# Performance work log

Measured on AMD Instinct MI355X. Metric: run time of the kernel, lower is better.

The kernel has to match this reference:

```python
import jax, jax.numpy as jnp
import numpy as np
from jax.scipy.special import logsumexp

EPS_OT = 0.05      # self.eps in AttentionOT
MAX_ITER = 100     # Sinkhorn max_iter (torch early-stops; at convergence results match)


def _l2norm(x):
    # F.normalize(x, dim=-1, p=2) with eps=1e-12
    return x / jnp.maximum(jnp.linalg.norm(x, axis=-1, keepdims=True), 1e-12)


def _sinkhorn(Cmat, mu, nu, eps):
    # Cmat: (BK, M, N), mu: (BK, M), nu: (BK, N)
    log_mu = jnp.log(mu + 1e-8)
    log_nu = jnp.log(nu + 1e-8)

    def kern(u, v):
        # log Boltzmann kernel: (-C + u_i + v_j) / eps, shape (BK, M, N)
        return (-Cmat + u[..., :, None] + v[..., None, :]) / eps

    def step(carry, _):
        u, v = carry
        u = eps * (log_mu - logsumexp(kern(u, v), axis=2)) + u
        v = eps * (log_nu - logsumexp(kern(u, v), axis=1)) + v
        return (u, v), None

    u0 = jnp.zeros_like(mu)
    v0 = jnp.zeros_like(nu)
    (u, v), _ = jax.lax.scan(jax.checkpoint(step), (u0, v0), None, length=MAX_ITER)
    return jnp.exp(kern(u, v))  # transport plan T, (BK, M, N)


def setup_inputs() -> dict:
    key = jax.random.key(0)
    Nq, M, B, K, C = 64, 16, 8, 256, 512
    ks = jax.random.split(key, 8)
    s = 1.0 / np.sqrt(C)  # torch nn.Linear default init bound
    return {
        "xq": jax.random.normal(ks[0], (Nq, M, B, C), jnp.float32),
        "xk": jax.random.normal(ks[1], (B, K, C), jnp.float32),
        "xv": jax.random.normal(ks[2], (B, K, C), jnp.float32),
        "Wq": jax.random.uniform(ks[3], (C, C), jnp.float32, -s, s),
        "Wk": jax.random.uniform(ks[4], (C, C), jnp.float32, -s, s),
        "Wv": jax.random.uniform(ks[5], (C, C), jnp.float32, -s, s),
        "Wp": jax.random.uniform(ks[6], (C, C), jnp.float32, -s, s),
        "bp": jax.random.uniform(ks[7], (C,), jnp.float32, -s, s),
    }


def reference(xq, xk, xv, Wq, Wk, Wv, Wp, bp):
    Nq, M, B, C = xq.shape
    K = xk.shape[1]
    # projections (qkv_bias=False; proj has bias). dropout probs are 0 -> identity.
    q = _l2norm(xq @ Wq.T)          # (Nq, M, B, C)
    kk = _l2norm(xk @ Wk.T)         # (B, K, C)
    v = xv @ Wv.T                   # (B, K, C)
    # torch: einsum('bkc,nmbc->bnkm') then permute(0,2,3,1) -> (B,K,M,Nq)
    sim = jnp.einsum('bkc,nmbc->bkmn', kk, q).reshape(B * K, M, Nq)
    wdist = 1.0 - sim
    mu = jnp.full((B * K, M), 1.0 / M, dtype=sim.dtype)
    nu = jnp.full((B * K, Nq), 1.0 / Nq, dtype=sim.dtype)
    T = _sinkhorn(wdist, mu, nu, EPS_OT)            # (B*K, M, Nq)
    score_map = (M * Nq * sim * T).reshape(B, K, M, Nq)
    attn = T.reshape(B, K, M, Nq).transpose(3, 0, 1, 2)  # (Nq, B, K, M)
    x = jnp.einsum('nbkm,bkc->nmbc', attn, v)            # (Nq, M, B, C)
    x = x @ Wp.T + bp
    return x, score_map
```

## Files before the change

kernel.cpp:

```cpp
#include <hip/hip_runtime.h>


typedef short   short8  __attribute__((ext_vector_type(8)));
typedef float   floatx4 __attribute__((ext_vector_type(4)));
typedef unsigned int uint2e __attribute__((ext_vector_type(2)));

static __device__ __forceinline__ float fastrcp(float x) {
    return __builtin_amdgcn_rcpf(x);
}
static __device__ __forceinline__ unsigned short f2bf(float f) {
    union { float f; unsigned u; } c; c.f = f;
    unsigned r = c.u + 0x7FFF + ((c.u >> 16) & 1);
    return (unsigned short)(r >> 16);
}
static __device__ __forceinline__ float bf2f(unsigned short h) {
    union { unsigned u; float f; } c; c.u = (unsigned)h << 16;
    return c.f;
}

static __device__ __forceinline__ void gll16(const unsigned short* g, short* l) {
    __builtin_amdgcn_global_load_lds(
        (const __attribute__((address_space(1))) void*)g,
        (__attribute__((address_space(3))) void*)l, 16, 0, 0);
}

#if __has_builtin(__builtin_amdgcn_permlane16_swap)
static __device__ __forceinline__ float xadd16(float s) {
    uint2e r = __builtin_amdgcn_permlane16_swap(
        __float_as_uint(s), __float_as_uint(s), false, false);
    return __uint_as_float(r.x) + __uint_as_float(r.y);
}
#else
static __device__ __forceinline__ float xadd16(float s) {
    return s + __shfl_xor(s, 16, 64);
}
#endif
#if __has_builtin(__builtin_amdgcn_permlane32_swap)
static __device__ __forceinline__ float xadd32(float s) {
    uint2e r = __builtin_amdgcn_permlane32_swap(
        __float_as_uint(s), __float_as_uint(s), false, false);
    return __uint_as_float(r.x) + __uint_as_float(r.y);
}
#else
static __device__ __forceinline__ float xadd32(float s) {
    return s + __shfl_xor(s, 32, 64);
}
#endif

#define RRI(x, C) __builtin_amdgcn_update_dpp(0, (x), (C), 0xf, 0xf, true)
#define RRF(x, C) __int_as_float(RRI(__float_as_int(x), (C)))
#define GATH16(d, s) do { d[0] = (s);                                        \
    d[1]  = RRF((s), 0x121); d[2]  = RRF((s), 0x122);                        \
    d[3]  = RRF((s), 0x123); d[4]  = RRF((s), 0x124);                        \
    d[5]  = RRF((s), 0x125); d[6]  = RRF((s), 0x126);                        \
    d[7]  = RRF((s), 0x127); d[8]  = RRF((s), 0x128);                        \
    d[9]  = RRF((s), 0x129); d[10] = RRF((s), 0x12a);                        \
    d[11] = RRF((s), 0x12b); d[12] = RRF((s), 0x12c);                        \
    d[13] = RRF((s), 0x12d); d[14] = RRF((s), 0x12e);                        \
    d[15] = RRF((s), 0x12f); } while (0)

__global__ __launch_bounds__(256) void prep(
    const float* __restrict__ xq, const float* __restrict__ xk,
    const float* __restrict__ xv, const float* __restrict__ Wq,
    const float* __restrict__ Wk, const float* __restrict__ Wv,
    const float* __restrict__ Wp,
    unsigned short* __restrict__ xqh, unsigned short* __restrict__ xql,
    unsigned short* __restrict__ xkh, unsigned short* __restrict__ xkl,
    unsigned short* __restrict__ xvb,
    unsigned short* __restrict__ wqh, unsigned short* __restrict__ wql,
    unsigned short* __restrict__ wkh, unsigned short* __restrict__ wkl,
    unsigned short* __restrict__ wvb, unsigned short* __restrict__ wpb)
{
    const int b = blockIdx.x;
    const float* src; unsigned short *dh, *dl; long base;
    if (b < 4096)      { src = xq; dh = xqh; dl = xql;     base = (long)b * 256; }
    else if (b < 5120) { src = xk; dh = xkh; dl = xkl;     base = (long)(b - 4096) * 256; }
    else if (b < 6144) { src = xv; dh = xvb; dl = nullptr; base = (long)(b - 5120) * 256; }
    else if (b < 6400) { src = Wq; dh = wqh; dl = wql;     base = (long)(b - 6144) * 256; }
    else if (b < 6656) { src = Wk; dh = wkh; dl = wkl;     base = (long)(b - 6400) * 256; }
    else if (b < 6912) { src = Wv; dh = wvb; dl = nullptr; base = (long)(b - 6656) * 256; }
    else               { src = Wp; dh = wpb; dl = nullptr; base = (long)(b - 6912) * 256; }
    const long i = base + threadIdx.x;
    float4 v = ((const float4*)src)[i];
    ushort4 h;
    h.x = f2bf(v.x); h.y = f2bf(v.y); h.z = f2bf(v.z); h.w = f2bf(v.w);
    ((ushort4*)dh)[i] = h;
    if (dl) {
        ushort4 l;
        l.x = f2bf(v.x - bf2f(h.x)); l.y = f2bf(v.y - bf2f(h.y));
        l.z = f2bf(v.z - bf2f(h.z)); l.w = f2bf(v.w - bf2f(h.w));
        ((ushort4*)dl)[i] = l;
    }
}

__global__ __launch_bounds__(256, 3) void gemm_qkv2(
    const unsigned short* __restrict__ xqh, const unsigned short* __restrict__ xql,
    const unsigned short* __restrict__ xkh, const unsigned short* __restrict__ xkl,
    const unsigned short* __restrict__ xvb,
    const unsigned short* __restrict__ wqh, const unsigned short* __restrict__ wql,
    const unsigned short* __restrict__ wkh, const unsigned short* __restrict__ wkl,
    const unsigned short* __restrict__ wvb,
    unsigned short* __restrict__ qh, unsigned short* __restrict__ ql,
    unsigned short* __restrict__ kh, unsigned short* __restrict__ kl,
    unsigned short* __restrict__ vt)
{
    __shared__ __align__(16) short LB[24576];

    const int bt = blockIdx.x;
    const unsigned short *Ah, *Al, *Bh, *Bl;
    int seg, arow0;
    if (bt < 128)      { Ah = xqh; Al = xql; Bh = wqh; Bl = wql; arow0 = bt * 64;         seg = 0; }
    else if (bt < 160) { Ah = xkh; Al = xkl; Bh = wkh; Bl = wkl; arow0 = (bt - 128) * 64; seg = 1; }
    else               { Ah = xvb; Al = xvb; Bh = wvb; Bl = wvb; arow0 = (bt - 160) * 64; seg = 2; }
    const bool split = (seg != 2);

    const int tid  = threadIdx.x;
    const int lane = tid & 63, wv = tid >> 6;
    const int wc = wv * 32;
    const int j0 = blockIdx.y * 128;

    floatx4 acc[4][2];
#pragma unroll
    for (int i = 0; i < 4; i++)
#pragma unroll
        for (int j = 0; j < 2; j++) acc[i][j] = {0.f, 0.f, 0.f, 0.f};

    const int lrow = lane >> 2;
    const int lch  = (lane & 3) * 8;
    const int gra  = 16 * wv;
    const int grb  = 32 * wv;
    const long gA0 = (long)(arow0 + gra + lrow) * 512 + lch;
    const long gB0 = (long)(j0    + grb + lrow) * 512 + lch;

    const int fr = lane & 15, fq = (lane >> 4) * 8;

#define QKV_STAGE(d, k0) do {                                                 \
        short* bb = LB + (d) * 12288;                                         \
        gll16(Ah + gA0 + (k0),            bb + gra * 32);                     \
        gll16(Bh + gB0 + (k0),            bb + 4096 + grb * 32);              \
        gll16(Bh + gB0 + (k0) + 16 * 512, bb + 4096 + (grb + 16) * 32);       \
        if (split) {                                                          \
            gll16(Al + gA0 + (k0),            bb + 2048 + gra * 32);          \
            gll16(Bl + gB0 + (k0),            bb + 8192 + grb * 32);          \
            gll16(Bl + gB0 + (k0) + 16 * 512, bb + 8192 + (grb + 16) * 32);   \
        }                                                                     \
    } while (0)

    QKV_STAGE(0, 0);
    __syncthreads();

#pragma unroll 2
    for (int t = 0; t < 16; t++) {
        const int cur = t & 1;
        if (t < 15) QKV_STAGE(cur ^ 1, (t + 1) * 32);
        const short* base = LB + cur * 12288;
        short8 ah[4], bh[2];
#pragma unroll
        for (int i = 0; i < 4; i++)
            ah[i] = *(const short8*)&base[(i * 16 + fr) * 32 + fq];
#pragma unroll
        for (int j = 0; j < 2; j++)
            bh[j] = *(const short8*)&base[4096 + (wc + j * 16 + fr) * 32 + fq];
        if (split) {
            short8 al[4], bl[2];
#pragma unroll
            for (int i = 0; i < 4; i++)
                al[i] = *(const short8*)&base[2048 + (i * 16 + fr) * 32 + fq];
#pragma unroll
            for (int j = 0; j < 2; j++)
                bl[j] = *(const short8*)&base[8192 + (wc + j * 16 + fr) * 32 + fq];
#pragma unroll
            for (int i = 0; i < 4; i++)
#pragma unroll
                for (int j = 0; j < 2; j++) {
                    acc[i][j] = __builtin_amdgcn_mfma_f32_16x16x32_bf16(ah[i], bh[j], acc[i][j], 0, 0, 0);
                    acc[i][j] = __builtin_amdgcn_mfma_f32_16x16x32_bf16(ah[i], bl[j], acc[i][j], 0, 0, 0);
                    acc[i][j] = __builtin_amdgcn_mfma_f32_16x16x32_bf16(al[i], bh[j], acc[i][j], 0, 0, 0);
                }
        } else {
#pragma unroll
            for (int i = 0; i < 4; i++)
#pragma unroll
                for (int j = 0; j < 2; j++)
                    acc[i][j] = __builtin_amdgcn_mfma_f32_16x16x32_bf16(ah[i], bh[j], acc[i][j], 0, 0, 0);
        }
        __syncthreads();
    }
#undef QKV_STAGE

    const int cr = (lane >> 4) * 4, cc = lane & 15;
    if (seg == 2) {
        short (*S2)[72] = (short(*)[72])LB;
#pragma unroll
        for (int i = 0; i < 4; i++)
#pragma unroll
            for (int j = 0; j < 2; j++)
#pragma unroll
                for (int r = 0; r < 4; r++)
                    S2[wc + j * 16 + cc][i * 16 + cr + r] =
                        (short)f2bf(acc[i][j][r]);
        __syncthreads();
        const int orow = tid >> 1;
        const int os   = (tid & 1) * 32;
        unsigned short* dst = vt + (long)(arow0 >> 8) * 131072
                            + (long)(j0 + orow) * 256 + (arow0 & 255) + os;
#pragma unroll
        for (int c8 = 0; c8 < 4; c8++)
            *(short8*)(dst + c8 * 8) = *(const short8*)&S2[orow][os + c8 * 8];
    } else {
#pragma unroll
        for (int i = 0; i < 4; i++)
#pragma unroll
            for (int j = 0; j < 2; j++) {
                const int gj = j0 + wc + j * 16 + cc;
#pragma unroll
                for (int r = 0; r < 4; r++) {
                    const int gi = arow0 + i * 16 + cr + r;
                    const float v = acc[i][j][r];
                    const unsigned short h = f2bf(v);
                    const unsigned short lo = f2bf(v - bf2f(h));
                    if (seg == 0) {
                        const long orow = (long)((gi & 7) * 1024 + ((gi >> 3) & 15) * 64 + (gi >> 7));
                        qh[orow * 512 + gj] = h;
                        ql[orow * 512 + gj] = lo;
                    } else {
                        kh[(long)gi * 512 + gj] = h;
                        kl[(long)gi * 512 + gj] = lo;
                    }
                }
            }
    }
}

__global__ __launch_bounds__(256) void gemm_sim64(
    const short* __restrict__ Ah, const short* __restrict__ Al,
    const short* __restrict__ Bh, const short* __restrict__ Bl,
    float* __restrict__ Out)
{
    const int z = blockIdx.z;
    Ah += (long)z * 131072;  Al += (long)z * 131072;
    Bh += (long)z * 524288;  Bl += (long)z * 524288;
    Out += (long)z * 262144;

    __shared__ __align__(16) short Ash[64][40];
    __shared__ __align__(16) short Asl[64][40];
    __shared__ __align__(16) short Bsh[64][40];
    __shared__ __align__(16) short Bsl[64][40];
    __shared__ float sRA[64];
    __shared__ float sRB[64];

    const int tid  = threadIdx.x;
    const int lane = tid & 63, wv = tid >> 6;
    const int wr = (wv >> 1) * 32, wc = (wv & 1) * 32;
    const int i0 = blockIdx.x * 64, j0 = blockIdx.y * 64;

    floatx4 acc[2][2];
#pragma unroll
    for (int i = 0; i < 2; i++)
#pragma unroll
        for (int j = 0; j < 2; j++) acc[i][j] = {0.f, 0.f, 0.f, 0.f};

    const int sr = tid >> 2, sch = (tid & 3) * 8;
    const int fr = lane & 15, fq = (lane >> 4) * 8;

    float ssqA = 0.0f, ssqB = 0.0f;

    for (int k0 = 0; k0 < 512; k0 += 32) {
        const long ao = (long)(i0 + sr) * 512 + k0 + sch;
        const long bo = (long)(j0 + sr) * 512 + k0 + sch;
        const short8 vah = *(const short8*)(Ah + ao);
        const short8 val_ = *(const short8*)(Al + ao);
        const short8 vbh = *(const short8*)(Bh + bo);
        const short8 vbl = *(const short8*)(Bl + bo);
        *(short8*)&Ash[sr][sch] = vah;
        *(short8*)&Asl[sr][sch] = val_;
        *(short8*)&Bsh[sr][sch] = vbh;
        *(short8*)&Bsl[sr][sch] = vbl;
#pragma unroll
        for (int e = 0; e < 8; e++) {
            const float va = bf2f((unsigned short)vah[e]) + bf2f((unsigned short)val_[e]);
            const float vb = bf2f((unsigned short)vbh[e]) + bf2f((unsigned short)vbl[e]);
            ssqA = fmaf(va, va, ssqA);
            ssqB = fmaf(vb, vb, ssqB);
        }
        __syncthreads();
        short8 ah[2], al[2], bh[2], bl[2];
#pragma unroll
        for (int i = 0; i < 2; i++) {
            ah[i] = *(const short8*)&Ash[wr + i * 16 + fr][fq];
            al[i] = *(const short8*)&Asl[wr + i * 16 + fr][fq];
        }
#pragma unroll
        for (int j = 0; j < 2; j++) {
            bh[j] = *(const short8*)&Bsh[wc + j * 16 + fr][fq];
            bl[j] = *(const short8*)&Bsl[wc + j * 16 + fr][fq];
        }
#pragma unroll
        for (int i = 0; i < 2; i++)
#pragma unroll
            for (int j = 0; j < 2; j++) {
                acc[i][j] = __builtin_amdgcn_mfma_f32_16x16x32_bf16(ah[i], bh[j], acc[i][j], 0, 0, 0);
                acc[i][j] = __builtin_amdgcn_mfma_f32_16x16x32_bf16(ah[i], bl[j], acc[i][j], 0, 0, 0);
                acc[i][j] = __builtin_amdgcn_mfma_f32_16x16x32_bf16(al[i], bh[j], acc[i][j], 0, 0, 0);
            }
        __syncthreads();
    }

    ssqA += __shfl_xor(ssqA, 1, 64);  ssqA += __shfl_xor(ssqA, 2, 64);
    ssqB += __shfl_xor(ssqB, 1, 64);  ssqB += __shfl_xor(ssqB, 2, 64);
    if ((tid & 3) == 0) {
        sRA[sr] = 1.0f / fmaxf(sqrtf(ssqA), 1e-12f);
        sRB[sr] = 1.0f / fmaxf(sqrtf(ssqB), 1e-12f);
    }
    __syncthreads();

    const int cr = (lane >> 4) * 4, cc = lane & 15;
#pragma unroll
    for (int i = 0; i < 2; i++)
#pragma unroll
        for (int j = 0; j < 2; j++) {
            const int lc = wc + j * 16 + cc;
            const float sq = sRB[lc];
            const int gj = j0 + lc;
#pragma unroll
            for (int r = 0; r < 4; r++) {
                const int lr = wr + i * 16 + cr + r;
                Out[(long)(i0 + lr) * 1024 + gj] = acc[i][j][r] * sRA[lr] * sq;
            }
        }
}

template <bool BIAS, bool OPERM, bool OUT_BF16>
__global__ __launch_bounds__(256, 2) void gemm_bf16_v2(
    const unsigned short* __restrict__ A, const unsigned short* __restrict__ B,
    const float* __restrict__ bias, void* __restrict__ OutV,
    int Kdim, int lda, int ldb, int ldo, long sA, long sB, long sO)
{
    __shared__ __align__(16) short LB[12288];

    const int tid  = threadIdx.x;
    const int lane = tid & 63, wv = tid >> 6;
    const int wc = wv * 32;
    const int i0 = blockIdx.x * 64, j0 = blockIdx.y * 128;

    floatx4 acc[4][2];
#pragma unroll
    for (int i = 0; i < 4; i++)
#pragma unroll
        for (int j = 0; j < 2; j++) acc[i][j] = {0.f, 0.f, 0.f, 0.f};

    const unsigned short* pa = A + (long)blockIdx.z * sA;
    const unsigned short* pb = B + (long)blockIdx.z * sB;

    const int lrow = lane >> 2;
    const int lch  = (lane & 3) * 8;
    const int gra  = 16 * wv;
    const int grb  = 32 * wv;
    const long gA0 = (long)(i0 + gra + lrow) * lda + lch;
    const long gB0 = (long)(j0 + grb + lrow) * ldb + lch;

    const int fr = lane & 15, fq = (lane >> 4) * 8;

#define BF2_STAGE(d, k0) do {                                                 \
        short* bb = LB + (d) * 6144;                                          \
        gll16(pa + gA0 + (k0),             bb + gra * 32);                    \
        gll16(pb + gB0 + (k0),             bb + 2048 + grb * 32);             \
        gll16(pb + gB0 + (k0) + 16 * ldb,  bb + 2048 + (grb + 16) * 32);      \
    } while (0)

    const int nt = Kdim >> 5;
    BF2_STAGE(0, 0);
    __syncthreads();

#pragma unroll 2
    for (int t = 0; t < nt; t++) {
        const int cur = t & 1;
        if (t < nt - 1) BF2_STAGE(cur ^ 1, (t + 1) * 32);
        const short* base = LB + cur * 6144;
        short8 af[4], bf[2];
#pragma unroll
        for (int i = 0; i < 4; i++)
            af[i] = *(const short8*)&base[(i * 16 + fr) * 32 + fq];
#pragma unroll
        for (int j = 0; j < 2; j++)
            bf[j] = *(const short8*)&base[2048 + (wc + j * 16 + fr) * 32 + fq];
#pragma unroll
        for (int i = 0; i < 4; i++)
#pragma unroll
            for (int j = 0; j < 2; j++)
                acc[i][j] = __builtin_amdgcn_mfma_f32_16x16x32_bf16(af[i], bf[j], acc[i][j], 0, 0, 0);
        __syncthreads();
    }
#undef BF2_STAGE

    float* Of = nullptr; unsigned short* Ob = nullptr;
    if constexpr (OUT_BF16) Ob = (unsigned short*)OutV + (long)blockIdx.z * sO;
    else                    Of = (float*)OutV + (long)blockIdx.z * sO;
    const int cr = (lane >> 4) * 4, cc = lane & 15;
#pragma unroll
    for (int i = 0; i < 4; i++) {
#pragma unroll
        for (int j = 0; j < 2; j++) {
            const int gj = j0 + wc + j * 16 + cc;
            float bb = 0.0f;
            if constexpr (BIAS) bb = bias[gj];
#pragma unroll
            for (int r = 0; r < 4; r++) {
                const int gi = i0 + i * 16 + cr + r;
                float v = acc[i][j][r] + bb;
                long idx;
                if constexpr (OPERM)
                    idx = (long)((gi & 63) * 128 + ((gi >> 6) & 15) * 8 + (gi >> 10)) * ldo + gj;
                else
                    idx = (long)gi * ldo + gj;
                if constexpr (OUT_BF16) Ob[idx] = f2bf(v);
                else                    Of[idx] = v;
            }
        }
    }
}

__global__ __launch_bounds__(256, 2) void sinkhorn5(
    const float* __restrict__ sim, float* __restrict__ score,
    unsigned short* __restrict__ Tt)
{
    const int lane = threadIdx.x & 63;
    const int bk   = blockIdx.x * 4 + (threadIdx.x >> 6);
    const float* S = sim + (long)bk * 1024;
    const int m = lane & 15, g = lane >> 4;

    int idx[16];
    idx[0] = m;
    idx[1]  = RRI(m, 0x121); idx[2]  = RRI(m, 0x122); idx[3]  = RRI(m, 0x123);
    idx[4]  = RRI(m, 0x124); idx[5]  = RRI(m, 0x125); idx[6]  = RRI(m, 0x126);
    idx[7]  = RRI(m, 0x127); idx[8]  = RRI(m, 0x128); idx[9]  = RRI(m, 0x129);
    idx[10] = RRI(m, 0x12a); idx[11] = RRI(m, 0x12b); idx[12] = RRI(m, 0x12c);
    idx[13] = RRI(m, 0x12d); idx[14] = RRI(m, 0x12e); idx[15] = RRI(m, 0x12f);

    float K1[16], K2R[16], sv[16];
#pragma unroll
    for (int j = 0; j < 16; j++) {
        K1[j] = __expf((S[m * 64 + g * 16 + idx[j]] - 1.0f) * 20.0f);
        const float s_ = S[idx[j] * 64 + lane];
        sv[j]  = s_;
        K2R[j] = __expf((s_ - 1.0f) * 20.0f);
    }

    const float muP = 0.0625f + 1e-8f;
    const float nuP = 0.015625f + 1e-8f;
    float b = 1.0f;
    float aB[16], bB[16];
#pragma unroll
    for (int j = 0; j < 16; j++) bB[j] = 1.0f;

#pragma unroll 1
    for (int it = 0; it < 100; it++) {
        float s0 = 0, s1 = 0, s2 = 0, s3 = 0;
#pragma unroll
        for (int j = 0; j < 4; j++) {
            s0 = fmaf(K1[j],      bB[j],      s0);
            s1 = fmaf(K1[4 + j],  bB[4 + j],  s1);
            s2 = fmaf(K1[8 + j],  bB[8 + j],  s2);
            s3 = fmaf(K1[12 + j], bB[12 + j], s3);
        }
        float s = (s0 + s1) + (s2 + s3);
        s = xadd16(s);
        s = xadd32(s);
        const float a = muP * fastrcp(s);
        GATH16(aB, a);
        float t0 = 0, t1 = 0, t2 = 0, t3 = 0;
#pragma unroll
        for (int j = 0; j < 4; j++) {
            t0 = fmaf(K2R[j],      aB[j],      t0);
            t1 = fmaf(K2R[4 + j],  aB[4 + j],  t1);
            t2 = fmaf(K2R[8 + j],  aB[8 + j],  t2);
            t3 = fmaf(K2R[12 + j], aB[12 + j], t3);
        }
        const float bp_ = b;
        b = nuP * fastrcp((t0 + t1) + (t2 + t3));
        GATH16(bB, b);
        const int conv = __builtin_fabsf(b - bp_) <= 1e-5f * __builtin_fabsf(b);
        if (__all(conv)) break;
    }

    float* Sc = score + (long)bk * 1024;
    unsigned short* Tp = Tt + (long)(bk >> 8) * 262144 + (bk & 255);
#pragma unroll
    for (int j = 0; j < 16; j++) {
        const int row = idx[j];
        const float Tv = aB[j] * K2R[j] * b;
        Sc[row * 64 + lane] = 1024.0f * sv[j] * Tv;
        Tp[(long)(row * 64 + lane) * 256] = f2bf(Tv);
    }
}

extern "C" void kernel_launch(void* const* d_in, const int* in_sizes, int n_in,
                              void* d_out, int out_size, void* d_ws, size_t ws_size,
                              hipStream_t stream)
{
    (void)in_sizes; (void)n_in; (void)out_size; (void)ws_size;
    const float* xq = (const float*)d_in[0];
    const float* xk = (const float*)d_in[1];
    const float* xv = (const float*)d_in[2];
    const float* Wq = (const float*)d_in[3];
    const float* Wk = (const float*)d_in[4];
    const float* Wv = (const float*)d_in[5];
    const float* Wp = (const float*)d_in[6];
    const float* bp = (const float*)d_in[7];

    float* out_x     = (float*)d_out;
    float* out_score = out_x + 8192L * 512;

    char* W = (char*)d_ws;
    const long MB = 1 << 20;
    unsigned short* qh   = (unsigned short*)(W + 0);
    unsigned short* ql   = (unsigned short*)(W + 8 * MB);
    unsigned short* xq_h = (unsigned short*)(W + 16 * MB);
    float*          simb = (float*)(W + 16 * MB);
    unsigned short* xq_l = (unsigned short*)(W + 24 * MB);
    unsigned short* xpre = (unsigned short*)(W + 24 * MB);
    unsigned short* xk_h = (unsigned short*)(W + 32 * MB);
    unsigned short* xk_l = (unsigned short*)(W + 34 * MB);
    unsigned short* Tt   = (unsigned short*)(W + 32 * MB);
    unsigned short* xv_b = (unsigned short*)(W + 36 * MB);
    unsigned short* kh   = (unsigned short*)(W + 38 * MB);
    unsigned short* kl   = (unsigned short*)(W + 40 * MB);
    unsigned short* vt   = (unsigned short*)(W + 42 * MB);
    unsigned short* wqh  = (unsigned short*)(W + 44 * MB);
    unsigned short* wql  = (unsigned short*)(W + 44 * MB + 1 * 524288);
    unsigned short* wkh  = (unsigned short*)(W + 44 * MB + 2 * 524288);
    unsigned short* wkl  = (unsigned short*)(W + 44 * MB + 3 * 524288);
    unsigned short* wvb  = (unsigned short*)(W + 44 * MB + 4 * 524288);
    unsigned short* wpb  = (unsigned short*)(W + 44 * MB + 5 * 524288);

    const dim3 blk(256);

    prep<<<7168, blk, 0, stream>>>(xq, xk, xv, Wq, Wk, Wv, Wp,
                                   xq_h, xq_l, xk_h, xk_l, xv_b,
                                   wqh, wql, wkh, wkl, wvb, wpb);

    gemm_qkv2<<<dim3(192, 4), blk, 0, stream>>>(
        xq_h, xq_l, xk_h, xk_l, xv_b, wqh, wql, wkh, wkl, wvb,
        qh, ql, kh, kl, vt);

    gemm_sim64<<<dim3(4, 16, 8), blk, 0, stream>>>(
        (const short*)kh, (const short*)kl, (const short*)qh, (const short*)ql,
        simb);

    sinkhorn5<<<512, blk, 0, stream>>>(simb, out_score, Tt);

    gemm_bf16_v2<false, false, true><<<dim3(16, 4, 8), blk, 0, stream>>>(
        Tt, vt, nullptr, xpre,
        256, 256, 256, 512, 262144, 131072, 524288);

    gemm_bf16_v2<true, true, false><<<dim3(128, 4), blk, 0, stream>>>(
        xpre, wpb, bp, out_x,
        512, 512, 512, 512, 0, 0, 0);
}
```

Before: 180.4 us.

## Fuse row norms into QKV epilogue and double-buffer sim GEMM with LDS DMA

The q and k row sums of squares now accumulate in the projection GEMM epilogue through shuffles and atomics into a buffer that prep zeroes. The sim GEMM therefore no longer computes them per tile. The sim GEMM also moves from register-staged LDS loads to global_load_lds direct loads with a double buffer, which lets loads overlap MFMA work. This adds atomic traffic and more LDS per block (launch bounds now allow 2 blocks). Each epilogue thread also recomputes rsqrt from global memory.

```diff
diff --git a/kernel.cpp b/kernel.cpp
--- a/kernel.cpp
+++ b/kernel.cpp
@@ -69,7 +69,8 @@
     unsigned short* __restrict__ xvb,
     unsigned short* __restrict__ wqh, unsigned short* __restrict__ wql,
     unsigned short* __restrict__ wkh, unsigned short* __restrict__ wkl,
-    unsigned short* __restrict__ wvb, unsigned short* __restrict__ wpb)
+    unsigned short* __restrict__ wvb, unsigned short* __restrict__ wpb,
+    float* __restrict__ rs)
 {
     const int b = blockIdx.x;
     const float* src; unsigned short *dh, *dl; long base;
@@ -91,6 +92,10 @@
         l.z = f2bf(v.z - bf2f(h.z)); l.w = f2bf(v.w - bf2f(h.w));
         ((ushort4*)dl)[i] = l;
     }
+    if (b == 7167) {
+#pragma unroll
+        for (int ii = 0; ii < 40; ii++) rs[threadIdx.x + ii * 256] = 0.0f;
+    }
 }
 
 __global__ __launch_bounds__(256, 3) void gemm_qkv2(
@@ -102,7 +107,7 @@
     const unsigned short* __restrict__ wvb,
     unsigned short* __restrict__ qh, unsigned short* __restrict__ ql,
     unsigned short* __restrict__ kh, unsigned short* __restrict__ kl,
-    unsigned short* __restrict__ vt)
+    unsigned short* __restrict__ vt, float* __restrict__ rs)
 {
     __shared__ __align__(16) short LB[24576];
 
@@ -208,6 +213,9 @@
         for (int c8 = 0; c8 < 4; c8++)
             *(short8*)(dst + c8 * 8) = *(const short8*)&S2[orow][os + c8 * 8];
     } else {
+        float prow[16];
+#pragma unroll
+        for (int ii = 0; ii < 16; ii++) prow[ii] = 0.0f;
 #pragma unroll
         for (int i = 0; i < 4; i++)
 #pragma unroll
@@ -219,6 +227,8 @@
                     const float v = acc[i][j][r];
                     const unsigned short h = f2bf(v);
                     const unsigned short lo = f2bf(v - bf2f(h));
+                    const float vv = bf2f(h) + bf2f(lo);
+                    prow[i * 4 + r] = fmaf(vv, vv, prow[i * 4 + r]);
                     if (seg == 0) {
                         const long orow = (long)((gi & 7) * 1024 + ((gi >> 3) & 15) * 64 + (gi >> 7));
                         qh[orow * 512 + gj] = h;
@@ -229,25 +239,41 @@
                     }
                 }
             }
-    }
-}
-
-__global__ __launch_bounds__(256) void gemm_sim64(
-    const short* __restrict__ Ah, const short* __restrict__ Al,
-    const short* __restrict__ Bh, const short* __restrict__ Bl,
-    float* __restrict__ Out)
+#pragma unroll
+        for (int i = 0; i < 4; i++)
+#pragma unroll
+            for (int r = 0; r < 4; r++) {
+                float p = prow[i * 4 + r];
+                p += __shfl_xor(p, 1, 64);
+                p += __shfl_xor(p, 2, 64);
+                p += __shfl_xor(p, 4, 64);
+                p += __shfl_xor(p, 8, 64);
+                if (cc == 0) {
+                    const int gi = arow0 + i * 16 + cr + r;
+                    long ri;
+                    if (seg == 0)
+                        ri = (long)((gi & 7) * 1024 + ((gi >> 3) & 15) * 64 + (gi >> 7));
+                    else
+                        ri = 8192 + (long)gi;
+                    atomicAdd(rs + ri, p);
+                }
+            }
+    }
+}
+
+__global__ __launch_bounds__(256, 2) void gemm_sim64(
+    const unsigned short* __restrict__ Ah, const unsigned short* __restrict__ Al,
+    const unsigned short* __restrict__ Bh, const unsigned short* __restrict__ Bl,
+    float* __restrict__ Out, const float* __restrict__ rs)
 {
     const int z = blockIdx.z;
     Ah += (long)z * 131072;  Al += (long)z * 131072;
     Bh += (long)z * 524288;  Bl += (long)z * 524288;
     Out += (long)z * 262144;
-
-    __shared__ __align__(16) short Ash[64][40];
-    __shared__ __align__(16) short Asl[64][40];
-    __shared__ __align__(16) short Bsh[64][40];
-    __shared__ __align__(16) short Bsl[64][40];
-    __shared__ float sRA[64];
-    __shared__ float sRB[64];
+    const float* rsq = rs + (long)z * 1024;
+    const float* rsk = rs + 8192 + (long)z * 256;
+
+    __shared__ __align__(16) short LB[16384];
 
     const int tid  = threadIdx.x;
     const int lane = tid & 63, wv = tid >> 6;
@@ -260,40 +286,40 @@
 #pragma unroll
         for (int j = 0; j < 2; j++) acc[i][j] = {0.f, 0.f, 0.f, 0.f};
 
-    const int sr = tid >> 2, sch = (tid & 3) * 8;
+    const int lrow = lane >> 2;
+    const int lch  = (lane & 3) * 8;
+    const int gr   = 16 * wv;
+    const long gA0 = (long)(i0 + gr + lrow) * 512 + lch;
+    const long gB0 = (long)(j0 + gr + lrow) * 512 + lch;
+
     const int fr = lane & 15, fq = (lane >> 4) * 8;
 
-    float ssqA = 0.0f, ssqB = 0.0f;
-
-    for (int k0 = 0; k0 < 512; k0 += 32) {
-        const long ao = (long)(i0 + sr) * 512 + k0 + sch;
-        const long bo = (long)(j0 + sr) * 512 + k0 + sch;
-        const short8 vah = *(const short8*)(Ah + ao);
-        const short8 val_ = *(const short8*)(Al + ao);
-        const short8 vbh = *(const short8*)(Bh + bo);
-        const short8 vbl = *(const short8*)(Bl + bo);
-        *(short8*)&Ash[sr][sch] = vah;
-        *(short8*)&Asl[sr][sch] = val_;
-        *(short8*)&Bsh[sr][sch] = vbh;
-        *(short8*)&Bsl[sr][sch] = vbl;
-#pragma unroll
-        for (int e = 0; e < 8; e++) {
-            const float va = bf2f((unsigned short)vah[e]) + bf2f((unsigned short)val_[e]);
-            const float vb = bf2f((unsigned short)vbh[e]) + bf2f((unsigned short)vbl[e]);
-            ssqA = fmaf(va, va, ssqA);
-            ssqB = fmaf(vb, vb, ssqB);
-        }
-        __syncthreads();
+#define SIM_STAGE(d, k0) do {                                                 \
+        short* bb = LB + (d) * 8192;                                          \
+        gll16(Ah + gA0 + (k0), bb + gr * 32);                                 \
+        gll16(Al + gA0 + (k0), bb + 2048 + gr * 32);                          \
+        gll16(Bh + gB0 + (k0), bb + 4096 + gr * 32);                          \
+        gll16(Bl + gB0 + (k0), bb + 6144 + gr * 32);                          \
+    } while (0)
+
+    SIM_STAGE(0, 0);
+    __syncthreads();
+
+#pragma unroll 2
+    for (int t = 0; t < 16; t++) {
+        const int cur = t & 1;
+        if (t < 15) SIM_STAGE(cur ^ 1, (t + 1) * 32);
+        const short* base = LB + cur * 8192;
         short8 ah[2], al[2], bh[2], bl[2];
 #pragma unroll
         for (int i = 0; i < 2; i++) {
-            ah[i] = *(const short8*)&Ash[wr + i * 16 + fr][fq];
-            al[i] = *(const short8*)&Asl[wr + i * 16 + fr][fq];
+            ah[i] = *(const short8*)&base[(wr + i * 16 + fr) * 32 + fq];
+            al[i] = *(const short8*)&base[2048 + (wr + i * 16 + fr) * 32 + fq];
         }
 #pragma unroll
         for (int j = 0; j < 2; j++) {
-            bh[j] = *(const short8*)&Bsh[wc + j * 16 + fr][fq];
-            bl[j] = *(const short8*)&Bsl[wc + j * 16 + fr][fq];
+            bh[j] = *(const short8*)&base[4096 + (wc + j * 16 + fr) * 32 + fq];
+            bl[j] = *(const short8*)&base[6144 + (wc + j * 16 + fr) * 32 + fq];
         }
 #pragma unroll
         for (int i = 0; i < 2; i++)
@@ -305,14 +331,7 @@
             }
         __syncthreads();
     }
-
-    ssqA += __shfl_xor(ssqA, 1, 64);  ssqA += __shfl_xor(ssqA, 2, 64);
-    ssqB += __shfl_xor(ssqB, 1, 64);  ssqB += __shfl_xor(ssqB, 2, 64);
-    if ((tid & 3) == 0) {
-        sRA[sr] = 1.0f / fmaxf(sqrtf(ssqA), 1e-12f);
-        sRB[sr] = 1.0f / fmaxf(sqrtf(ssqB), 1e-12f);
-    }
-    __syncthreads();
+#undef SIM_STAGE
 
     const int cr = (lane >> 4) * 4, cc = lane & 15;
 #pragma unroll
@@ -320,12 +339,13 @@
 #pragma unroll
         for (int j = 0; j < 2; j++) {
             const int lc = wc + j * 16 + cc;
-            const float sq = sRB[lc];
+            const float sq = 1.0f / fmaxf(sqrtf(rsq[j0 + lc]), 1e-12f);
             const int gj = j0 + lc;
 #pragma unroll
             for (int r = 0; r < 4; r++) {
                 const int lr = wr + i * 16 + cr + r;
-                Out[(long)(i0 + lr) * 1024 + gj] = acc[i][j][r] * sRA[lr] * sq;
+                const float sa = 1.0f / fmaxf(sqrtf(rsk[i0 + lr]), 1e-12f);
+                Out[(long)(i0 + lr) * 1024 + gj] = acc[i][j][r] * sa * sq;
             }
         }
 }
@@ -532,20 +552,22 @@
     unsigned short* wkl  = (unsigned short*)(W + 44 * MB + 3 * 524288);
     unsigned short* wvb  = (unsigned short*)(W + 44 * MB + 4 * 524288);
     unsigned short* wpb  = (unsigned short*)(W + 44 * MB + 5 * 524288);
+    float*          rs   = (float*)(W + 47 * MB);
 
     const dim3 blk(256);
 
     prep<<<7168, blk, 0, stream>>>(xq, xk, xv, Wq, Wk, Wv, Wp,
                                    xq_h, xq_l, xk_h, xk_l, xv_b,
-                                   wqh, wql, wkh, wkl, wvb, wpb);
+                                   wqh, wql, wkh, wkl, wvb, wpb, rs);
 
     gemm_qkv2<<<dim3(192, 4), blk, 0, stream>>>(
         xq_h, xq_l, xk_h, xk_l, xv_b, wqh, wql, wkh, wkl, wvb,
-        qh, ql, kh, kl, vt);
+        qh, ql, kh, kl, vt, rs);
 
     gemm_sim64<<<dim3(4, 16, 8), blk, 0, stream>>>(
-        (const short*)kh, (const short*)kl, (const short*)qh, (const short*)ql,
-        simb);
+        xq_h ? (const unsigned short*)kh : nullptr, (const unsigned short*)kl,
+        (const unsigned short*)qh, (const unsigned short*)ql,
+        simb, rs);
 
     sinkhorn5<<<512, blk, 0, stream>>>(simb, out_score, Tt);
 
```

Result: slower. 185.4 us (+2.8%).
